# Performance work log

Measured on AMD Instinct MI355X. Metric: run time of the kernel, lower is better.

The kernel has to match this reference:

```python
import jax, jax.numpy as jnp
import numpy as np

DIM = 192          # out_dim
HEADS = 8          # num_heads (split into 2 branches of 4)
SS = (4, 8)        # split_size
B, HH, WW, CIN = 8, 128, 128, 192


def calc_mask(H, W, wh, ww):
    # Swin-style shift mask for windows of (wh, ww), shift (wh//2, ww//2).
    sh, sw = wh // 2, ww // 2
    h = jnp.arange(H)
    w = jnp.arange(W)
    hreg = (h >= H - wh).astype(jnp.int32) + (h >= H - sh).astype(jnp.int32)
    wreg = (w >= W - ww).astype(jnp.int32) + (w >= W - sw).astype(jnp.int32)
    img = hreg[:, None] * 3 + wreg[None, :]                      # (H, W) region ids
    win = img.reshape(H // wh, wh, W // ww, ww).transpose(0, 2, 1, 3).reshape(-1, wh * ww)
    return jnp.where(win[:, :, None] != win[:, None, :], -100.0, 0.0)  # (nW, N, N)


def window_attention(q, k, v, mask, d, Hsp, Wsp):
    # q,k,v: (B, C, H, W); mask: (u*v, N, N); d heads, window Hsp x Wsp
    Bc, C, H, W = k.shape
    u, vv = H // Hsp, W // Wsp
    c = C // d
    N = Hsp * Wsp
    scale = c ** -0.5

    def v2w(t):  # 'b (d c) (u h) (v w) -> (b u v) d (h w) c'
        return t.reshape(Bc, d, c, u, Hsp, vv, Wsp).transpose(0, 3, 5, 1, 4, 6, 2).reshape(Bc * u * vv, d, N, c)

    qw, kw, vw = v2w(q), v2w(k), v2w(v)
    attn = jnp.einsum('ndic,ndjc->ndij', qw, kw) * scale          # (B*u*v, d, N, N)
    attn = attn.reshape(Bc, u * vv, d, N, N) + mask[None, :, None, :, :]
    a = jax.nn.softmax(attn, axis=-1).reshape(Bc * u * vv, d, N, N)
    o = jnp.einsum('ndij,ndjc->ndic', a, vw)
    # '(b u v) d (h w) c -> b (d c) (u h) (v w)'
    return o.reshape(Bc, u, vv, d, Hsp, Wsp, c).transpose(0, 3, 6, 1, 4, 2, 5).reshape(Bc, C, H, W)


def setup_inputs() -> dict:
    key = jax.random.key(0)
    k0, k1, k2, k3 = jax.random.split(key, 4)
    x = jax.random.normal(k0, (B, HH * WW, CIN), dtype=jnp.float32)
    Wq = jax.random.normal(k1, (CIN, DIM), dtype=jnp.float32) * 0.02
    Wkv = jax.random.normal(k2, (CIN, 2 * DIM), dtype=jnp.float32) * 0.02
    Wproj = jax.random.normal(k3, (DIM, DIM), dtype=jnp.float32) * 0.02
    bproj = jnp.zeros((DIM,), dtype=jnp.float32)
    return {"x": x, "Wq": Wq, "Wkv": Wkv, "Wproj": Wproj, "bproj": bproj, "H": HH, "W": WW}


def reference(x, Wq, Wkv, Wproj, bproj, H, W):
    Bc, L, _ = x.shape
    C = Wq.shape[1]
    q = (x @ Wq).reshape(Bc, H, W, C).transpose(0, 3, 1, 2)       # (B, C, H, W)
    kv = (x @ Wkv).reshape(Bc, H, W, 2, C)
    k = kv[..., 0, :].transpose(0, 3, 1, 2)
    v = kv[..., 1, :].transpose(0, 3, 1, 2)

    Ch = C // 2
    s0, s1 = SS[0] // 2, SS[1] // 2
    roll0 = lambda t: jnp.roll(t, (-s0, -s1), axis=(-2, -1))
    roll1 = lambda t: jnp.roll(t, (-s1, -s0), axis=(-2, -1))
    mask0 = calc_mask(H, W, SS[0], SS[1])   # branch 0: 4x8 windows
    mask1 = calc_mask(H, W, SS[1], SS[0])   # branch 1: 8x4 windows
    d = HEADS // 2

    x0 = window_attention(roll0(q[:, :Ch]), roll0(k[:, :Ch]), roll0(v[:, :Ch]), mask0, d, SS[0], SS[1])
    x1 = window_attention(roll1(q[:, Ch:]), roll1(k[:, Ch:]), roll1(v[:, Ch:]), mask1, d, SS[1], SS[0])
    x0 = jnp.roll(x0, (s0, s1), axis=(-2, -1))
    x1 = jnp.roll(x1, (s1, s0), axis=(-2, -1))

    out = jnp.concatenate([x0, x1], axis=1)                        # (B, C, H, W)
    out = out.transpose(0, 2, 3, 1).reshape(Bc, L, C)
    return out @ Wproj + bproj
```

## Files before the change

kernel.cpp:

```cpp
#include <hip/hip_runtime.h>
#include <hip/hip_bf16.h>
#include <stdint.h>

typedef __bf16 bf16;
typedef __bf16 bf16x8 __attribute__((ext_vector_type(8)));
typedef __bf16 bf16x4 __attribute__((ext_vector_type(4)));
typedef float  f32x4  __attribute__((ext_vector_type(4)));

#define MROWS 131072

__device__ __forceinline__ f32x4 mfma16(bf16x8 a, bf16x8 b, f32x4 c) {
    return __builtin_amdgcn_mfma_f32_16x16x32_bf16(a, b, c, 0, 0, 0);
}
__device__ __forceinline__ f32x4 zero4() {
    f32x4 z; z[0]=0.f; z[1]=0.f; z[2]=0.f; z[3]=0.f; return z;
}
__device__ __forceinline__ bf16x8 zero8() {
    bf16x8 z;
#pragma unroll
    for (int i = 0; i < 8; ++i) z[i] = (bf16)0.f;
    return z;
}
template <int CTRL>
__device__ __forceinline__ float rowror(float x) {
    return __int_as_float(
        __builtin_amdgcn_mov_dpp(__float_as_int(x), CTRL, 0xF, 0xF, false));
}
__device__ __forceinline__ float rowmax16(float m) {
    m = fmaxf(m, rowror<0x128>(m));
    m = fmaxf(m, rowror<0x124>(m));
    m = fmaxf(m, rowror<0x122>(m));
    m = fmaxf(m, rowror<0x121>(m));
    return m;
}
__device__ __forceinline__ float rowsum16(float s) {
    s += rowror<0x128>(s);
    s += rowror<0x124>(s);
    s += rowror<0x122>(s);
    s += rowror<0x121>(s);
    return s;
}

__global__ void kw_transpose(const float* __restrict__ Wq, const float* __restrict__ Wkv,
                             const float* __restrict__ Wp, bf16* __restrict__ Wt,
                             bf16* __restrict__ Wpt) {
    int col = blockIdx.x;
    int k = threadIdx.x;
    if (col < 192)      Wt[col * 192 + k] = (bf16)Wq[k * 192 + col];
    else if (col < 576) Wt[col * 192 + k] = (bf16)Wkv[k * 384 + (col - 192)];
    else                Wpt[(col - 576) * 192 + k] = (bf16)Wp[k * 192 + (col - 576)];
}

__global__ __launch_bounds__(256, 4) void kfused(const float* __restrict__ X,
                                                 const bf16* __restrict__ Wt,
                                                 bf16* __restrict__ Out) {
    const int branch = blockIdx.y;
    const int bw = blockIdx.x;
    const int img = bw >> 9;
    const int widx = bw & 511;
    const int wh = branch ? 8 : 4, ww = branch ? 4 : 8;
    const int lww = branch ? 2 : 3;
    const int lnv = branch ? 5 : 4;
    const int sh = wh >> 1, sw = ww >> 1;
    const int wa = widx >> lnv;
    const int wb = widx & ((128 >> lww) - 1);

    __shared__ __align__(16) char smem[27136];
    bf16 (*xs)[200]    = (bf16(*)[200])smem;
    bf16 (*kss)[104]   = (bf16(*)[104])smem;
    bf16 (*pl)[32][40] = (bf16(*)[32][40])smem;
    bf16 (*qs)[104]    = (bf16(*)[104])(smem + 12800);
    bf16 (*ob)[104]    = (bf16(*)[104])(smem + 12800);
    bf16 (*vt)[24][40] = (bf16(*)[24][40])(smem + 19456);
    __shared__ int pix[32];
    __shared__ int rid[32];

    const int tid = threadIdx.x;
    if (tid < 32) {
        int ih = tid >> lww, iw = tid & (ww - 1);
        int hh = wa * wh + ih, wp = wb * ww + iw;
        int hreg = (hh >= 128 - wh) + (hh >= 128 - sh);
        int wreg = (wp >= 128 - ww) + (wp >= 128 - sw);
        rid[tid] = hreg * 3 + wreg;
        int srh = (hh + sh) & 127, srw = (wp + sw) & 127;
        pix[tid] = img * 16384 + srh * 128 + srw;
    }

    {
        int row = tid / 48, rem = tid % 48;
#pragma unroll
        for (int i = 0; i < 6; ++i) {
            int c4 = rem * 4;
            int ih = row >> lww, iw = row & (ww - 1);
            int hh = wa * wh + ih, wp = wb * ww + iw;
            int srh = (hh + sh) & 127, srw = (wp + sw) & 127;
            f32x4 f = *(const f32x4*)(X + (size_t)(img * 16384 + srh * 128 + srw) * 192 + c4);
            bf16x4 h;
#pragma unroll
            for (int e = 0; e < 4; ++e) h[e] = (bf16)f[e];
            *(bf16x4*)&xs[row][c4] = h;
            row += 5; rem += 16;
            if (rem >= 48) { rem -= 48; ++row; }
        }
    }
    __syncthreads();

    const int hd = tid >> 6;
    const int l = tid & 63, li = l & 15, lk = l >> 4;

    bf16x8 xf[2][6];
#pragma unroll
    for (int mt = 0; mt < 2; ++mt)
#pragma unroll
        for (int ks = 0; ks < 6; ++ks)
            xf[mt][ks] = *(const bf16x8*)&xs[mt * 16 + li][ks * 32 + lk * 8];

#define LOADW(dst, nt) {                                                            \
        int seg_ = (nt) / 6, cwi_ = ((nt) % 6) * 16;                                \
        const bf16* wr = Wt + (size_t)(seg_ * 192 + branch * 96 + cwi_ + li) * 192  \
                            + lk * 8;                                               \
        _Pragma("unroll")                                                           \
        for (int ks = 0; ks < 6; ++ks) dst[ks] = *(const bf16x8*)(wr + ks * 32);    \
    }
#define MFMA_SCATTER(frag, nt) {                                                    \
        f32x4 a0 = zero4(), a1 = zero4();                                           \
        _Pragma("unroll")                                                           \
        for (int ks = 0; ks < 6; ++ks) {                                            \
            a0 = mfma16(frag[ks], xf[0][ks], a0);                                   \
            a1 = mfma16(frag[ks], xf[1][ks], a1);                                   \
        }                                                                           \
        int seg_ = (nt) / 6, cwi_ = ((nt) % 6) * 16;                                \
        if (seg_ < 2) {                                                             \
            bf16 (*dst)[104] = (seg_ == 0) ? qs : kss;                              \
            bf16x4 p0, p1;                                                          \
            _Pragma("unroll")                                                       \
            for (int r = 0; r < 4; ++r) { p0[r] = (bf16)a0[r]; p1[r] = (bf16)a1[r]; } \
            *(bf16x4*)&dst[li][cwi_ + lk * 4] = p0;                                 \
            *(bf16x4*)&dst[16 + li][cwi_ + lk * 4] = p1;                            \
        } else {                                                                    \
            _Pragma("unroll")                                                       \
            for (int r = 0; r < 4; ++r) {                                           \
                int vc = cwi_ + lk * 4 + r;                                         \
                vt[vc / 24][vc % 24][li] = (bf16)a0[r];                             \
                vt[vc / 24][vc % 24][16 + li] = (bf16)a1[r];                        \
            }                                                                       \
        }                                                                           \
    }

    bf16x8 cur[6], nxt[6];
    LOADW(cur, hd);
    __syncthreads();

#pragma unroll
    for (int j = 0; j < 4; ++j) {
        int nt = hd + 4 * j;
        if (j < 3) {
            LOADW(nxt, nt + 4);
        } else if (hd < 2) {
            LOADW(nxt, nt + 4);
        }
        MFMA_SCATTER(cur, nt);
#pragma unroll
        for (int ks = 0; ks < 6; ++ks) cur[ks] = nxt[ks];
    }
    if (hd < 2) {
        MFMA_SCATTER(cur, hd + 16);
    }
    __syncthreads();

    bf16x8 aq[2], bk[2];
#pragma unroll
    for (int t = 0; t < 2; ++t) {
        if (lk < 3) {
            aq[t] = *(const bf16x8*)&qs[t * 16 + li][hd * 24 + lk * 8];
            bk[t] = *(const bf16x8*)&kss[t * 16 + li][hd * 24 + lk * 8];
        } else {
            aq[t] = zero8();
            bk[t] = zero8();
        }
    }
    f32x4 s[2][2];
#pragma unroll
    for (int it = 0; it < 2; ++it)
#pragma unroll
        for (int jt = 0; jt < 2; ++jt) s[it][jt] = mfma16(aq[it], bk[jt], zero4());

    __syncthreads();

    const float scale = 0.2041241452319315f;
    const int r0 = lk * 4;
    const int rj0 = rid[li], rj1 = rid[16 + li];
#pragma unroll
    for (int it = 0; it < 2; ++it) {
#pragma unroll
        for (int r = 0; r < 4; ++r) {
            int i = it * 16 + r0 + r;
            int ri = rid[i];
            float v0 = s[it][0][r] * scale + ((ri != rj0) ? -100.f : 0.f);
            float v1 = s[it][1][r] * scale + ((ri != rj1) ? -100.f : 0.f);
            float m = rowmax16(fmaxf(v0, v1));
            float e0 = __expf(v0 - m), e1 = __expf(v1 - m);
            float sm = rowsum16(e0 + e1);
            float inv = 1.f / sm;
            pl[hd][i][li] = (bf16)(e0 * inv);
            pl[hd][i][16 + li] = (bf16)(e1 * inv);
        }
    }
    __syncthreads();

    bf16x8 ap[2], bv[2];
#pragma unroll
    for (int it = 0; it < 2; ++it)
        ap[it] = *(const bf16x8*)(&pl[hd][it * 16 + li][lk * 8]);
#pragma unroll
    for (int ct = 0; ct < 2; ++ct) {
        int col = ct * 16 + li;
        if (col > 23) col = 23;
        bv[ct] = *(const bf16x8*)(&vt[hd][col][lk * 8]);
    }
    f32x4 o[2][2];
#pragma unroll
    for (int it = 0; it < 2; ++it)
#pragma unroll
        for (int ct = 0; ct < 2; ++ct) o[it][ct] = mfma16(ap[it], bv[ct], zero4());

#pragma unroll
    for (int it = 0; it < 2; ++it)
#pragma unroll
        for (int ct = 0; ct < 2; ++ct) {
            int col = ct * 16 + li;
            if (col < 24) {
#pragma unroll
                for (int r = 0; r < 4; ++r)
                    ob[it * 16 + r0 + r][hd * 24 + col] = (bf16)o[it][ct][r];
            }
        }
    __syncthreads();
    for (int c = tid; c < 384; c += 256) {
        int row = c / 12, ch = c % 12;
        *(bf16x8*)(Out + (size_t)pix[row] * 192 + branch * 96 + ch * 8) =
            *(const bf16x8*)&ob[row][ch * 8];
    }
#undef LOADW
#undef MFMA_SCATTER
}

#define BSTR 200
__global__ __launch_bounds__(256, 4) void kproj(const bf16* __restrict__ Ab,
                                                const bf16* __restrict__ Wpt,
                                                const float* __restrict__ bias,
                                                float* __restrict__ Out) {
    __shared__ __align__(16) bf16 Bs[96][BSTR];
    const int lid = blockIdx.x;
    const int xcd = lid & 7, s = lid >> 3;
    const int mg = xcd * 128 + s / 2;
    const int nb = s & 1;
    const int tid = threadIdx.x;
    const int w = tid >> 6, l = tid & 63, li = l & 15, lk = l >> 4;
    const int rb = mg * 128 + w * 32;
    const int cb = nb * 96;

    bf16x8 a[2][6];
#pragma unroll
    for (int it = 0; it < 2; ++it)
#pragma unroll
        for (int ks = 0; ks < 6; ++ks)
            a[it][ks] = *(const bf16x8*)(Ab + (size_t)(rb + it * 16 + li) * 192 + ks * 32 + lk * 8);

#pragma unroll
    for (int i = 0; i < 9; ++i) {
        int c = i * 256 + tid;
        int r = c / 24, col = (c % 24) * 8;
        *(bf16x8*)&Bs[r][col] = *(const bf16x8*)(Wpt + (size_t)(cb + r) * 192 + col);
    }
    __syncthreads();

    f32x4 acc[2][6];
#pragma unroll
    for (int it = 0; it < 2; ++it)
#pragma unroll
        for (int nt = 0; nt < 6; ++nt) acc[it][nt] = zero4();

#pragma unroll
    for (int nt = 0; nt < 6; ++nt) {
#pragma unroll
        for (int ks = 0; ks < 6; ++ks) {
            bf16x8 b = *(const bf16x8*)&Bs[nt * 16 + li][ks * 32 + lk * 8];
            acc[0][nt] = mfma16(b, a[0][ks], acc[0][nt]);
            acc[1][nt] = mfma16(b, a[1][ks], acc[1][nt]);
        }
    }

#pragma unroll
    for (int nt = 0; nt < 6; ++nt) {
        f32x4 bv4 = *(const f32x4*)(bias + cb + nt * 16 + lk * 4);
#pragma unroll
        for (int it = 0; it < 2; ++it) {
            f32x4 ov = acc[it][nt];
#pragma unroll
            for (int r = 0; r < 4; ++r) ov[r] += bv4[r];
            *(f32x4*)(Out + (size_t)(rb + it * 16 + li) * 192 + cb + nt * 16 + lk * 4) = ov;
        }
    }
}

extern "C" void kernel_launch(void* const* d_in, const int* in_sizes, int n_in,
                              void* d_out, int out_size, void* d_ws, size_t ws_size,
                              hipStream_t stream) {
    const float* x    = (const float*)d_in[0];
    const float* Wq   = (const float*)d_in[1];
    const float* Wkv  = (const float*)d_in[2];
    const float* Wp   = (const float*)d_in[3];
    const float* bias = (const float*)d_in[4];
    float* out = (float*)d_out;

    bf16* Ab  = (bf16*)d_ws;
    bf16* Wt  = Ab + (size_t)MROWS * 192;
    bf16* Wpt = Wt + 576 * 192;

    hipLaunchKernelGGL(kw_transpose, dim3(768), dim3(192), 0, stream, Wq, Wkv, Wp, Wt, Wpt);
    hipLaunchKernelGGL(kfused, dim3(4096, 2), dim3(256), 0, stream, x, Wt, Ab);
    hipLaunchKernelGGL(kproj, dim3(2048), dim3(256), 0, stream, Ab, Wpt, bias, out);
}
```

Before: 146.3 us.

## Give each wave its own head's QKV projection to drop block barriers

Reorders the packed weights so every head's Q, K and V columns sit together, padded from 24 to 32 columns. Each wave then projects only its own head into a private shared-memory region, which removes the block-wide barriers between projection, scores, softmax and PV. This also evens out the work across waves, which were previously unbalanced at 4 or 5 tiles each. In exchange it does a third more MFMA work because of the zero padding, and shared memory per block grows, which may lower occupancy.

```diff
diff --git a/kernel.cpp b/kernel.cpp
--- a/kernel.cpp
+++ b/kernel.cpp
@@ -14,12 +14,6 @@
 }
 __device__ __forceinline__ f32x4 zero4() {
     f32x4 z; z[0]=0.f; z[1]=0.f; z[2]=0.f; z[3]=0.f; return z;
-}
-__device__ __forceinline__ bf16x8 zero8() {
-    bf16x8 z;
-#pragma unroll
-    for (int i = 0; i < 8; ++i) z[i] = (bf16)0.f;
-    return z;
 }
 template <int CTRL>
 __device__ __forceinline__ float rowror(float x) {
@@ -42,17 +36,31 @@
 }
 
 __global__ void kw_transpose(const float* __restrict__ Wq, const float* __restrict__ Wkv,
-                             const float* __restrict__ Wp, bf16* __restrict__ Wt,
+                             const float* __restrict__ Wp, bf16* __restrict__ Wt2,
                              bf16* __restrict__ Wpt) {
-    int col = blockIdx.x;
+    int id = blockIdx.x;
     int k = threadIdx.x;
-    if (col < 192)      Wt[col * 192 + k] = (bf16)Wq[k * 192 + col];
-    else if (col < 576) Wt[col * 192 + k] = (bf16)Wkv[k * 384 + (col - 192)];
-    else                Wpt[(col - 576) * 192 + k] = (bf16)Wp[k * 192 + (col - 576)];
+    if (id < 768) {
+        int col = id & 31;
+        int hd  = (id >> 5) & 3;
+        int seg = (id >> 7) % 3;
+        int br  = id / 384;
+        bf16 v = (bf16)0.f;
+        if (col < 24) {
+            int gc = br * 96 + hd * 24 + col;
+            if (seg == 0)      v = (bf16)Wq[k * 192 + gc];
+            else if (seg == 1) v = (bf16)Wkv[k * 384 + gc];
+            else               v = (bf16)Wkv[k * 384 + 192 + gc];
+        }
+        Wt2[(size_t)id * 192 + k] = v;
+    } else {
+        int col = id - 768;
+        Wpt[(size_t)col * 192 + k] = (bf16)Wp[k * 192 + col];
+    }
 }
 
 __global__ __launch_bounds__(256, 4) void kfused(const float* __restrict__ X,
-                                                 const bf16* __restrict__ Wt,
+                                                 const bf16* __restrict__ Wt2,
                                                  bf16* __restrict__ Out) {
     const int branch = blockIdx.y;
     const int bw = blockIdx.x;
@@ -65,17 +73,22 @@
     const int wa = widx >> lnv;
     const int wb = widx & ((128 >> lww) - 1);
 
-    __shared__ __align__(16) char smem[27136];
-    bf16 (*xs)[200]    = (bf16(*)[200])smem;
-    bf16 (*kss)[104]   = (bf16(*)[104])smem;
-    bf16 (*pl)[32][40] = (bf16(*)[32][40])smem;
-    bf16 (*qs)[104]    = (bf16(*)[104])(smem + 12800);
-    bf16 (*ob)[104]    = (bf16(*)[104])(smem + 12800);
-    bf16 (*vt)[24][40] = (bf16(*)[24][40])(smem + 19456);
+    __shared__ __align__(16) char smem[37376];
     __shared__ int pix[32];
     __shared__ int rid[32];
 
     const int tid = threadIdx.x;
+    const int hd = tid >> 6;
+    const int l = tid & 63, li = l & 15, lk = l >> 4;
+
+    bf16 (*xs)[200] = (bf16(*)[200])smem;
+    char* wbase = smem + hd * 7680;
+    bf16 (*Q)[40]  = (bf16(*)[40])wbase;
+    bf16 (*K)[40]  = (bf16(*)[40])(wbase + 2560);
+    bf16 (*VT)[40] = (bf16(*)[40])(wbase + 5120);
+    bf16 (*PL)[40] = Q;
+    bf16 (*ob)[104] = (bf16(*)[104])(smem + 30720);
+
     if (tid < 32) {
         int ih = tid >> lww, iw = tid & (ww - 1);
         int hh = wa * wh + ih, wp = wb * ww + iw;
@@ -105,9 +118,6 @@
     }
     __syncthreads();
 
-    const int hd = tid >> 6;
-    const int l = tid & 63, li = l & 15, lk = l >> 4;
-
     bf16x8 xf[2][6];
 #pragma unroll
     for (int mt = 0; mt < 2; ++mt)
@@ -115,77 +125,59 @@
         for (int ks = 0; ks < 6; ++ks)
             xf[mt][ks] = *(const bf16x8*)&xs[mt * 16 + li][ks * 32 + lk * 8];
 
-#define LOADW(dst, nt) {                                                            \
-        int seg_ = (nt) / 6, cwi_ = ((nt) % 6) * 16;                                \
-        const bf16* wr = Wt + (size_t)(seg_ * 192 + branch * 96 + cwi_ + li) * 192  \
-                            + lk * 8;                                               \
+#define LOADW(dst, seg_, t_) {                                                      \
+        const bf16* wr = Wt2 + ((size_t)((branch * 3 + (seg_)) * 4 + hd) * 32       \
+                                + (t_) * 16 + li) * 192 + lk * 8;                   \
         _Pragma("unroll")                                                           \
         for (int ks = 0; ks < 6; ++ks) dst[ks] = *(const bf16x8*)(wr + ks * 32);    \
     }
-#define MFMA_SCATTER(frag, nt) {                                                    \
-        f32x4 a0 = zero4(), a1 = zero4();                                           \
-        _Pragma("unroll")                                                           \
-        for (int ks = 0; ks < 6; ++ks) {                                            \
-            a0 = mfma16(frag[ks], xf[0][ks], a0);                                   \
-            a1 = mfma16(frag[ks], xf[1][ks], a1);                                   \
-        }                                                                           \
-        int seg_ = (nt) / 6, cwi_ = ((nt) % 6) * 16;                                \
-        if (seg_ < 2) {                                                             \
-            bf16 (*dst)[104] = (seg_ == 0) ? qs : kss;                              \
-            bf16x4 p0, p1;                                                          \
-            _Pragma("unroll")                                                       \
-            for (int r = 0; r < 4; ++r) { p0[r] = (bf16)a0[r]; p1[r] = (bf16)a1[r]; } \
-            *(bf16x4*)&dst[li][cwi_ + lk * 4] = p0;                                 \
-            *(bf16x4*)&dst[16 + li][cwi_ + lk * 4] = p1;                            \
-        } else {                                                                    \
-            _Pragma("unroll")                                                       \
-            for (int r = 0; r < 4; ++r) {                                           \
-                int vc = cwi_ + lk * 4 + r;                                         \
-                vt[vc / 24][vc % 24][li] = (bf16)a0[r];                             \
-                vt[vc / 24][vc % 24][16 + li] = (bf16)a1[r];                        \
-            }                                                                       \
-        }                                                                           \
-    }
 
     bf16x8 cur[6], nxt[6];
-    LOADW(cur, hd);
+    LOADW(cur, 0, 0);
     __syncthreads();
 
 #pragma unroll
-    for (int j = 0; j < 4; ++j) {
-        int nt = hd + 4 * j;
-        if (j < 3) {
-            LOADW(nxt, nt + 4);
-        } else if (hd < 2) {
-            LOADW(nxt, nt + 4);
-        }
-        MFMA_SCATTER(cur, nt);
+    for (int j = 0; j < 6; ++j) {
+        if (j < 5) {
+            const int jn = j + 1;
+            LOADW(nxt, jn >> 1, jn & 1);
+        }
+        f32x4 a0 = zero4(), a1 = zero4();
+#pragma unroll
+        for (int ks = 0; ks < 6; ++ks) {
+            a0 = mfma16(cur[ks], xf[0][ks], a0);
+            a1 = mfma16(cur[ks], xf[1][ks], a1);
+        }
+        const int seg = j >> 1, t = j & 1;
+        if (seg < 2) {
+            bf16 (*dst)[40] = seg ? K : Q;
+            bf16x4 p0, p1;
+#pragma unroll
+            for (int r = 0; r < 4; ++r) { p0[r] = (bf16)a0[r]; p1[r] = (bf16)a1[r]; }
+            *(bf16x4*)&dst[li][t * 16 + lk * 4] = p0;
+            *(bf16x4*)&dst[16 + li][t * 16 + lk * 4] = p1;
+        } else {
+#pragma unroll
+            for (int r = 0; r < 4; ++r) {
+                VT[t * 16 + lk * 4 + r][li] = (bf16)a0[r];
+                VT[t * 16 + lk * 4 + r][16 + li] = (bf16)a1[r];
+            }
+        }
 #pragma unroll
         for (int ks = 0; ks < 6; ++ks) cur[ks] = nxt[ks];
     }
-    if (hd < 2) {
-        MFMA_SCATTER(cur, hd + 16);
-    }
-    __syncthreads();
 
     bf16x8 aq[2], bk[2];
 #pragma unroll
     for (int t = 0; t < 2; ++t) {
-        if (lk < 3) {
-            aq[t] = *(const bf16x8*)&qs[t * 16 + li][hd * 24 + lk * 8];
-            bk[t] = *(const bf16x8*)&kss[t * 16 + li][hd * 24 + lk * 8];
-        } else {
-            aq[t] = zero8();
-            bk[t] = zero8();
-        }
+        aq[t] = *(const bf16x8*)&Q[t * 16 + li][lk * 8];
+        bk[t] = *(const bf16x8*)&K[t * 16 + li][lk * 8];
     }
     f32x4 s[2][2];
 #pragma unroll
     for (int it = 0; it < 2; ++it)
 #pragma unroll
         for (int jt = 0; jt < 2; ++jt) s[it][jt] = mfma16(aq[it], bk[jt], zero4());
-
-    __syncthreads();
 
     const float scale = 0.2041241452319315f;
     const int r0 = lk * 4;
@@ -202,22 +194,18 @@
             float e0 = __expf(v0 - m), e1 = __expf(v1 - m);
             float sm = rowsum16(e0 + e1);
             float inv = 1.f / sm;
-            pl[hd][i][li] = (bf16)(e0 * inv);
-            pl[hd][i][16 + li] = (bf16)(e1 * inv);
-        }
-    }
-    __syncthreads();
+            PL[i][li] = (bf16)(e0 * inv);
+            PL[i][16 + li] = (bf16)(e1 * inv);
+        }
+    }
 
     bf16x8 ap[2], bv[2];
 #pragma unroll
     for (int it = 0; it < 2; ++it)
-        ap[it] = *(const bf16x8*)(&pl[hd][it * 16 + li][lk * 8]);
-#pragma unroll
-    for (int ct = 0; ct < 2; ++ct) {
-        int col = ct * 16 + li;
-        if (col > 23) col = 23;
-        bv[ct] = *(const bf16x8*)(&vt[hd][col][lk * 8]);
-    }
+        ap[it] = *(const bf16x8*)&PL[it * 16 + li][lk * 8];
+#pragma unroll
+    for (int ct = 0; ct < 2; ++ct)
+        bv[ct] = *(const bf16x8*)&VT[ct * 16 + li][lk * 8];
     f32x4 o[2][2];
 #pragma unroll
     for (int it = 0; it < 2; ++it)
@@ -242,7 +230,6 @@
             *(const bf16x8*)&ob[row][ch * 8];
     }
 #undef LOADW
-#undef MFMA_SCATTER
 }
 
 #define BSTR 200
@@ -315,10 +302,10 @@
     float* out = (float*)d_out;
 
     bf16* Ab  = (bf16*)d_ws;
-    bf16* Wt  = Ab + (size_t)MROWS * 192;
-    bf16* Wpt = Wt + 576 * 192;
-
-    hipLaunchKernelGGL(kw_transpose, dim3(768), dim3(192), 0, stream, Wq, Wkv, Wp, Wt, Wpt);
-    hipLaunchKernelGGL(kfused, dim3(4096, 2), dim3(256), 0, stream, x, Wt, Ab);
+    bf16* Wt2 = Ab + (size_t)MROWS * 192;
+    bf16* Wpt = Wt2 + 768 * 192;
+
+    hipLaunchKernelGGL(kw_transpose, dim3(960), dim3(192), 0, stream, Wq, Wkv, Wp, Wt2, Wpt);
+    hipLaunchKernelGGL(kfused, dim3(4096, 2), dim3(256), 0, stream, x, Wt2, Ab);
     hipLaunchKernelGGL(kproj, dim3(2048), dim3(256), 0, stream, Ab, Wpt, bias, out);
 }
```

After: 176.4 us. +20.6%, slower.

## Load X fragments directly into registers and interleave branches across blocks

Applied to the files above, without the earlier changes.

The input tile is now read from global memory straight into MFMA register fragments, skipping the LDS staging buffer and its barrier. The LDS layout is reorganized so the softmax probabilities no longer alias the other buffers, which removes one __syncthreads. The two branches are interleaved in a 1D grid so that adjacent blocks handle both branches of the same pixels, which may improve L2 reuse of X. In exchange every head-wave reloads the full X tile from global memory (four times the traffic, likely absorbed by cache), and LDS use grows, which could reduce occupancy.

```diff
diff --git a/kernel.cpp b/kernel.cpp
--- a/kernel.cpp
+++ b/kernel.cpp
@@ -54,8 +54,9 @@
 __global__ __launch_bounds__(256, 4) void kfused(const float* __restrict__ X,
                                                  const bf16* __restrict__ Wt,
                                                  bf16* __restrict__ Out) {
-    const int branch = blockIdx.y;
-    const int bw = blockIdx.x;
+    const int bid = blockIdx.x;
+    const int branch = bid & 1;
+    const int bw = bid >> 1;
     const int img = bw >> 9;
     const int widx = bw & 511;
     const int wh = branch ? 8 : 4, ww = branch ? 4 : 8;
@@ -65,17 +66,19 @@
     const int wa = widx >> lnv;
     const int wb = widx & ((128 >> lww) - 1);
 
-    __shared__ __align__(16) char smem[27136];
-    bf16 (*xs)[200]    = (bf16(*)[200])smem;
-    bf16 (*kss)[104]   = (bf16(*)[104])smem;
-    bf16 (*pl)[32][40] = (bf16(*)[32][40])smem;
-    bf16 (*qs)[104]    = (bf16(*)[104])(smem + 12800);
-    bf16 (*ob)[104]    = (bf16(*)[104])(smem + 12800);
-    bf16 (*vt)[24][40] = (bf16(*)[24][40])(smem + 19456);
+    __shared__ __align__(16) char smem[31232];
+    bf16 (*qs)[104]    = (bf16(*)[104])smem;
+    bf16 (*ob)[104]    = (bf16(*)[104])smem;
+    bf16 (*kss)[104]   = (bf16(*)[104])(smem + 6656);
+    bf16 (*vt)[24][40] = (bf16(*)[24][40])(smem + 13312);
+    bf16 (*pl)[32][40] = (bf16(*)[32][40])(smem + 20992);
     __shared__ int pix[32];
     __shared__ int rid[32];
 
     const int tid = threadIdx.x;
+    const int hd = tid >> 6;
+    const int l = tid & 63, li = l & 15, lk = l >> 4;
+
     if (tid < 32) {
         int ih = tid >> lww, iw = tid & (ww - 1);
         int hh = wa * wh + ih, wp = wb * ww + iw;
@@ -86,35 +89,6 @@
         pix[tid] = img * 16384 + srh * 128 + srw;
     }
 
-    {
-        int row = tid / 48, rem = tid % 48;
-#pragma unroll
-        for (int i = 0; i < 6; ++i) {
-            int c4 = rem * 4;
-            int ih = row >> lww, iw = row & (ww - 1);
-            int hh = wa * wh + ih, wp = wb * ww + iw;
-            int srh = (hh + sh) & 127, srw = (wp + sw) & 127;
-            f32x4 f = *(const f32x4*)(X + (size_t)(img * 16384 + srh * 128 + srw) * 192 + c4);
-            bf16x4 h;
-#pragma unroll
-            for (int e = 0; e < 4; ++e) h[e] = (bf16)f[e];
-            *(bf16x4*)&xs[row][c4] = h;
-            row += 5; rem += 16;
-            if (rem >= 48) { rem -= 48; ++row; }
-        }
-    }
-    __syncthreads();
-
-    const int hd = tid >> 6;
-    const int l = tid & 63, li = l & 15, lk = l >> 4;
-
-    bf16x8 xf[2][6];
-#pragma unroll
-    for (int mt = 0; mt < 2; ++mt)
-#pragma unroll
-        for (int ks = 0; ks < 6; ++ks)
-            xf[mt][ks] = *(const bf16x8*)&xs[mt * 16 + li][ks * 32 + lk * 8];
-
 #define LOADW(dst, nt) {                                                            \
         int seg_ = (nt) / 6, cwi_ = ((nt) % 6) * 16;                                \
         const bf16* wr = Wt + (size_t)(seg_ * 192 + branch * 96 + cwi_ + li) * 192  \
@@ -122,6 +96,33 @@
         _Pragma("unroll")                                                           \
         for (int ks = 0; ks < 6; ++ks) dst[ks] = *(const bf16x8*)(wr + ks * 32);    \
     }
+
+    bf16x8 cur[6], nxt[6];
+    LOADW(cur, hd);
+
+    bf16x8 xf[2][6];
+#pragma unroll
+    for (int mt = 0; mt < 2; ++mt) {
+        int row = mt * 16 + li;
+        int ih = row >> lww, iw = row & (ww - 1);
+        int hh = wa * wh + ih, wp = wb * ww + iw;
+        int srh = (hh + sh) & 127, srw = (wp + sw) & 127;
+        const float* xr = X + (size_t)(img * 16384 + srh * 128 + srw) * 192 + lk * 8;
+        f32x4 f0[6], f1[6];
+#pragma unroll
+        for (int ks = 0; ks < 6; ++ks) {
+            f0[ks] = *(const f32x4*)(xr + ks * 32);
+            f1[ks] = *(const f32x4*)(xr + ks * 32 + 4);
+        }
+#pragma unroll
+        for (int ks = 0; ks < 6; ++ks) {
+            bf16x8 v;
+#pragma unroll
+            for (int e = 0; e < 4; ++e) { v[e] = (bf16)f0[ks][e]; v[4 + e] = (bf16)f1[ks][e]; }
+            xf[mt][ks] = v;
+        }
+    }
+
 #define MFMA_SCATTER(frag, nt) {                                                    \
         f32x4 a0 = zero4(), a1 = zero4();                                           \
         _Pragma("unroll")                                                           \
@@ -147,10 +148,6 @@
         }                                                                           \
     }
 
-    bf16x8 cur[6], nxt[6];
-    LOADW(cur, hd);
-    __syncthreads();
-
 #pragma unroll
     for (int j = 0; j < 4; ++j) {
         int nt = hd + 4 * j;
@@ -206,17 +203,16 @@
             pl[hd][i][16 + li] = (bf16)(e1 * inv);
         }
     }
-    __syncthreads();
 
     bf16x8 ap[2], bv[2];
 #pragma unroll
     for (int it = 0; it < 2; ++it)
-        ap[it] = *(const bf16x8*)(&pl[hd][it * 16 + li][lk * 8]);
+        ap[it] = *(const bf16x8*)&pl[hd][it * 16 + li][lk * 8];
 #pragma unroll
     for (int ct = 0; ct < 2; ++ct) {
         int col = ct * 16 + li;
         if (col > 23) col = 23;
-        bv[ct] = *(const bf16x8*)(&vt[hd][col][lk * 8]);
+        bv[ct] = *(const bf16x8*)&vt[hd][col][lk * 8];
     }
     f32x4 o[2][2];
 #pragma unroll
@@ -319,6 +315,6 @@
     bf16* Wpt = Wt + 576 * 192;
 
     hipLaunchKernelGGL(kw_transpose, dim3(768), dim3(192), 0, stream, Wq, Wkv, Wp, Wt, Wpt);
-    hipLaunchKernelGGL(kfused, dim3(4096, 2), dim3(256), 0, stream, x, Wt, Ab);
+    hipLaunchKernelGGL(kfused, dim3(8192), dim3(256), 0, stream, x, Wt, Ab);
     hipLaunchKernelGGL(kproj, dim3(2048), dim3(256), 0, stream, Ab, Wpt, bias, out);
 }
```

Result: slower. 220.9 us (+51.0%).
